# Kernel tuning notes

Measured on AMD Instinct MI355X. Metric: run time of the kernel, lower is better.

## Reference

```python
import jax, jax.numpy as jnp
import numpy as np

B, N, C, H = 32, 512, 1024, 16
HD = C // H  # head_dim = 64
SCALE = HD ** -0.5


def setup_inputs() -> dict:
    key = jax.random.key(0)
    k1, k2, k3, k4 = jax.random.split(key, 4)
    # xavier_uniform bounds
    qkv_bound = (6.0 / (C + 3 * C)) ** 0.5
    proj_bound = 1.414 * (6.0 / (C + C)) ** 0.5
    return {
        "x": jax.random.normal(k1, (B, N, C), dtype=jnp.float32),
        "mask": jax.random.uniform(k2, (B, N), dtype=jnp.float32),
        "W_qkv": jax.random.uniform(k3, (3 * C, C), dtype=jnp.float32, minval=-qkv_bound, maxval=qkv_bound),
        "W_proj": jax.random.uniform(k4, (C, C), dtype=jnp.float32, minval=-proj_bound, maxval=proj_bound),
        "b_proj": jnp.zeros((C,), dtype=jnp.float32),
    }


def reference(x, mask, W_qkv, W_proj, b_proj):
    # qkv projection (no bias): [B,N,3C] -> [3,B,H,N,HD]
    qkv = jnp.einsum("bnc,dc->bnd", x, W_qkv)
    qkv = qkv.reshape(B, N, 3, H, HD).transpose(2, 0, 3, 1, 4)
    q, k, v = qkv[0] * SCALE, qkv[1], qkv[2]
    # attention scores [B,H,N,N] with additive row/col mask bias
    attn = jnp.einsum("bhqd,bhkd->bhqk", q, k)
    attn = attn + mask[:, None, None, :] + mask[:, None, :, None]
    attn = jax.nn.softmax(attn, axis=-1)
    out = jnp.einsum("bhqk,bhkd->bhqd", attn, v)
    out = out.transpose(0, 2, 1, 3).reshape(B, N, C)
    return jnp.einsum("bnc,dc->bnd", out, W_proj) + b_proj
```

## Files before the change

kernel.cpp:

```cpp
#include <hip/hip_runtime.h>
#include <stdint.h>

typedef unsigned short u16;
typedef __bf16 bf16x8 __attribute__((ext_vector_type(8)));
typedef float  f32x4  __attribute__((ext_vector_type(4)));
typedef float  f32x16 __attribute__((ext_vector_type(16)));
typedef unsigned int u32x4 __attribute__((ext_vector_type(4)));

#define MFMA16(a,b,c) __builtin_amdgcn_mfma_f32_16x16x32_bf16((a),(b),(c),0,0,0)
#define MFMA32(a,b,c) __builtin_amdgcn_mfma_f32_32x32x16_bf16((a),(b),(c),0,0,0)

#if __has_builtin(__builtin_amdgcn_exp2f)
#define EXP2F(x) __builtin_amdgcn_exp2f(x)
#else
#define EXP2F(x) exp2f(x)
#endif

__device__ __forceinline__ u16 f2b(float f) {
  unsigned int u = __builtin_bit_cast(unsigned int, f);
  u += 0x7fffu + ((u >> 16) & 1u);
  return (u16)(u >> 16);
}

__device__ __forceinline__ void gll16(const u16* g, u16* l) {
  __builtin_amdgcn_global_load_lds((const __attribute__((address_space(1))) unsigned int*)g,
                                   (__attribute__((address_space(3))) unsigned int*)l,
                                   16, 0, 0);
}

__device__ __forceinline__ unsigned cvtpk(float lo, float hi) {
  unsigned r;
  asm("v_cvt_pk_bf16_f32 %0, %1, %2" : "=v"(r) : "v"(lo), "v"(hi));
  return r;
}
__device__ __forceinline__ void pl32swap(unsigned &x, unsigned &y) {
  asm volatile("v_permlane32_swap_b32 %0, %1" : "+v"(x), "+v"(y));
}

__global__ __launch_bounds__(256)
void cvt_all(const float* __restrict__ X, const float* __restrict__ Wq,
             const float* __restrict__ Wp, u16* __restrict__ Xb,
             u16* __restrict__ Wqb, u16* __restrict__ Wpb)
{
  size_t i = (size_t)blockIdx.x * 256 + threadIdx.x;
  const float* src; u16* dst; size_t off;
  if (i < 4194304)       { src = X;  dst = Xb;  off = i; }
  else if (i < 4980736)  { src = Wq; dst = Wqb; off = i - 4194304; }
  else                   { src = Wp; dst = Wpb; off = i - 4980736; }
  float4 v = ((const float4*)src)[off];
  uint2 p;
  p.x = f2b(v.x) | ((unsigned)f2b(v.y) << 16);
  p.y = f2b(v.z) | ((unsigned)f2b(v.w) << 16);
  ((uint2*)dst)[off] = p;
}

__global__ __launch_bounds__(256, 2)
void qkv_gemm(const u16* __restrict__ Xb, const u16* __restrict__ Wb,
              u16* __restrict__ qb, u16* __restrict__ kb, u16* __restrict__ vT)
{
  __shared__ u16 As[128 * 32];
  __shared__ u16 Bs[128 * 32];
  const int t = threadIdx.x;
  const int row0 = blockIdx.y * 128;
  const int col0 = blockIdx.x * 128;
  const int lane = t & 63, w = t >> 6;
  const int quad = lane >> 4, l16 = lane & 15;
  const int wm = w & 1, wn = w >> 1;

  f32x4 acc[4][4];
#pragma unroll
  for (int i = 0; i < 4; i++)
#pragma unroll
    for (int j = 0; j < 4; j++) acc[i][j] = f32x4{0.f, 0.f, 0.f, 0.f};

  const int srow = lane >> 2;
  const int kpart = (lane & 3) ^ ((lane >> 3) & 3);
  const u16* ga[2]; const u16* gb[2];
  u16* la[2]; u16* lb[2];
#pragma unroll
  for (int j = 0; j < 2; j++) {
    int r = w * 32 + j * 16 + srow;
    ga[j] = Xb + (size_t)(row0 + r) * 1024 + kpart * 8;
    gb[j] = Wb + (size_t)(col0 + r) * 1024 + kpart * 8;
    la[j] = As + (w * 2 + j) * 512;
    lb[j] = Bs + (w * 2 + j) * 512;
  }

  int aoff[4], boff[4];
#pragma unroll
  for (int mt = 0; mt < 4; mt++) { int r = wm * 64 + mt * 16 + l16; aoff[mt] = r * 64 + ((quad ^ ((r >> 1) & 3)) * 16); }
#pragma unroll
  for (int nt = 0; nt < 4; nt++) { int r = wn * 64 + nt * 16 + l16; boff[nt] = r * 64 + ((quad ^ ((r >> 1) & 3)) * 16); }

  for (int k0 = 0; k0 < 1024; k0 += 32) {
    __syncthreads();
#pragma unroll
    for (int j = 0; j < 2; j++) {
      gll16(ga[j] + k0, la[j]);
      gll16(gb[j] + k0, lb[j]);
    }
    __syncthreads();
    bf16x8 af[4], bfr[4];
#pragma unroll
    for (int mt = 0; mt < 4; mt++) af[mt] = *(const bf16x8*)((const char*)As + aoff[mt]);
#pragma unroll
    for (int nt = 0; nt < 4; nt++) bfr[nt] = *(const bf16x8*)((const char*)Bs + boff[nt]);
#pragma unroll
    for (int mt = 0; mt < 4; mt++)
#pragma unroll
      for (int nt = 0; nt < 4; nt++)
        acc[mt][nt] = MFMA16(af[mt], bfr[nt], acc[mt][nt]);
  }

  const int tok_base = row0 + wm * 64;
#pragma unroll
  for (int nt = 0; nt < 4; nt++) {
    int d = col0 + wn * 64 + nt * 16;
    int part = d >> 10;
    int hh = (d >> 6) & 15;
    int hd = (d & 63) + l16;
    if (part == 2) {
#pragma unroll
      for (int mt = 0; mt < 4; mt++) {
        int nb = tok_base + mt * 16 + quad * 4;
        int bb = nb >> 9, nn = nb & 511;
        uint2 pk;
        pk.x = f2b(acc[mt][nt][0]) | ((unsigned)f2b(acc[mt][nt][1]) << 16);
        pk.y = f2b(acc[mt][nt][2]) | ((unsigned)f2b(acc[mt][nt][3]) << 16);
        *(uint2*)(vT + (((size_t)(bb * 16 + hh)) * 64 + hd) * 512 + nn) = pk;
      }
    } else {
      u16* dst = (part == 0) ? qb : kb;
      float sc = (part == 0) ? 0.125f : 1.0f;
#pragma unroll
      for (int mt = 0; mt < 4; mt++)
#pragma unroll
        for (int r = 0; r < 4; r++) {
          int tok = tok_base + mt * 16 + quad * 4 + r;
          int bb = tok >> 9, nn = tok & 511;
          dst[(((size_t)(bb * 16 + hh)) * 512 + nn) * 64 + hd] = f2b(acc[mt][nt][r] * sc);
        }
    }
  }
}

__global__ __launch_bounds__(256)
void attn_kernel(const u16* __restrict__ qb, const u16* __restrict__ kb,
                 const u16* __restrict__ vT, const float* __restrict__ mask,
                 u16* __restrict__ ao)
{
  __shared__ u16 Kbuf[2][64 * 64];
  __shared__ u16 Vbuf[2][64 * 64];
  __shared__ float mk2[512];
  __shared__ float Lbuf[128];

  const int bid = blockIdx.x;
  const int wid = (bid & 7) * 256 + (bid >> 3);
  const int qt = wid & 3, bh = wid >> 2;
  const int b = bh >> 4, hh = bh & 15;

  const int t = threadIdx.x;
  const int lane = t & 63, w = t >> 6;
  const int l31 = lane & 31, hi = lane >> 5;
  const int sw = l31 & 7;

  const u16* Qp = qb + (size_t)bh * 512 * 64;
  const u16* Kp = kb + (size_t)bh * 512 * 64;
  const u16* Vp = vT + (size_t)bh * 64 * 512;

  for (int i = t; i < 512; i += 256) mk2[i] = mask[b * 512 + i] * 1.44269504f;

  const int qbase = qt * 128 + w * 32;
  bf16x8 qf[4];
#pragma unroll
  for (int dc = 0; dc < 4; dc++)
    qf[dc] = *(const bf16x8*)(Qp + (size_t)(qbase + l31) * 64 + dc * 16 + hi * 8);

  const int sr = lane >> 3, sc = lane & 7;
  const int cg = sc ^ sr;
  const u16* gk[2]; const u16* gv[2];
#pragma unroll
  for (int j = 0; j < 2; j++) {
    int r = w * 16 + j * 8 + sr;
    gk[j] = Kp + (size_t)r * 64 + cg * 8;
    gv[j] = Vp + (size_t)r * 512 + cg * 8;
  }

  f32x16 oacc[2];
#pragma unroll
  for (int i = 0; i < 16; i++) { oacc[0][i] = 0.f; oacc[1][i] = 0.f; }
  float lsum = 0.f;

  auto STAGE = [&](int tt, int buf) {
#pragma unroll
    for (int j = 0; j < 2; j++) {
      gll16(gk[j] + (size_t)tt * 4096, &Kbuf[buf][(w * 16 + j * 8) * 64]);
      gll16(gv[j] + (size_t)tt * 64,   &Vbuf[buf][(w * 16 + j * 8) * 64]);
    }
  };

  STAGE(0, 0);
  __syncthreads();

  for (int tt = 0; tt < 8; tt++) {
    const int cur = tt & 1;
    if (tt < 7) STAGE(tt + 1, cur ^ 1);
    const u16* Kb = Kbuf[cur];
    const u16* Vb = Vbuf[cur];
#pragma unroll
    for (int c = 0; c < 2; c++) {
      f32x16 s;
#pragma unroll
      for (int i = 0; i < 16; i++) s[i] = 0.f;
#pragma unroll
      for (int dc = 0; dc < 4; dc++) {
        int row = c * 32 + l31;
        bf16x8 kf = *(const bf16x8*)((const char*)Kb + row * 128 + (((2 * dc + hi) ^ sw) * 16));
        s = MFMA32(kf, qf[dc], s);
      }
      const int kb0 = tt * 64 + c * 32;
      f32x4 mkv[4];
#pragma unroll
      for (int g = 0; g < 4; g++) mkv[g] = *(const f32x4*)(mk2 + kb0 + g * 8 + hi * 4);
      float p[16];
#pragma unroll
      for (int r = 0; r < 16; r++)
        p[r] = EXP2F(fmaf(s[r], 1.44269504f, mkv[r >> 2][r & 3]));
      float ls = 0.f;
#pragma unroll
      for (int r = 0; r < 16; r++) ls += p[r];
      lsum += ls;

      unsigned d0a = cvtpk(p[0],  p[1]),  d1a = cvtpk(p[2],  p[3]);
      unsigned d2a = cvtpk(p[4],  p[5]),  d3a = cvtpk(p[6],  p[7]);
      unsigned d0b = cvtpk(p[8],  p[9]),  d1b = cvtpk(p[10], p[11]);
      unsigned d2b = cvtpk(p[12], p[13]), d3b = cvtpk(p[14], p[15]);
      pl32swap(d0a, d2a);
      pl32swap(d1a, d3a);
      pl32swap(d0b, d2b);
      pl32swap(d1b, d3b);
      u32x4 w0; w0.x = d0a; w0.y = d1a; w0.z = d2a; w0.w = d3a;
      u32x4 w1; w1.x = d0b; w1.y = d1b; w1.z = d2b; w1.w = d3b;
      bf16x8 af[2];
      af[0] = __builtin_bit_cast(bf16x8, w0);
      af[1] = __builtin_bit_cast(bf16x8, w1);

#pragma unroll
      for (int kc = 0; kc < 2; kc++)
#pragma unroll
        for (int dc = 0; dc < 2; dc++) {
          int row = dc * 32 + l31;
          bf16x8 vf = *(const bf16x8*)((const char*)Vb + row * 128 + (((4 * c + 2 * kc + hi) ^ sw) * 16));
          oacc[dc] = MFMA32(af[kc], vf, oacc[dc]);
        }
    }
    __syncthreads();
  }

  lsum += __shfl_xor(lsum, 32);
  if (lane < 32) Lbuf[w * 32 + l31] = 1.0f / lsum;
  __syncthreads();
  f32x4 inv4[4];
#pragma unroll
  for (int g = 0; g < 4; g++) inv4[g] = *(const f32x4*)(Lbuf + w * 32 + g * 8 + hi * 4);

#pragma unroll
  for (int dc = 0; dc < 2; dc++)
#pragma unroll
    for (int r = 0; r < 16; r++) {
      int qrow = (r & 3) + 8 * (r >> 2) + 4 * hi;
      int n = qbase + qrow;
      int col = hh * 64 + dc * 32 + l31;
      ao[((size_t)(b * 512 + n)) * 1024 + col] = f2b(oacc[dc][r] * inv4[r >> 2][r & 3]);
    }
}

__global__ __launch_bounds__(256, 2)
void proj_gemm(const u16* __restrict__ A, const u16* __restrict__ Wb,
               const float* __restrict__ bias, float* __restrict__ out)
{
  __shared__ u16 As[128 * 32];
  __shared__ u16 Bs[128 * 32];
  const int t = threadIdx.x;
  const int row0 = blockIdx.y * 128;
  const int col0 = blockIdx.x * 128;
  const int lane = t & 63, w = t >> 6;
  const int quad = lane >> 4, l16 = lane & 15;
  const int wm = w & 1, wn = w >> 1;

  f32x4 acc[4][4];
#pragma unroll
  for (int i = 0; i < 4; i++)
#pragma unroll
    for (int j = 0; j < 4; j++) acc[i][j] = f32x4{0.f, 0.f, 0.f, 0.f};

  const int srow = lane >> 2;
  const int kpart = (lane & 3) ^ ((lane >> 3) & 3);
  const u16* ga[2]; const u16* gb[2];
  u16* la[2]; u16* lb[2];
#pragma unroll
  for (int j = 0; j < 2; j++) {
    int r = w * 32 + j * 16 + srow;
    ga[j] = A  + (size_t)(row0 + r) * 1024 + kpart * 8;
    gb[j] = Wb + (size_t)(col0 + r) * 1024 + kpart * 8;
    la[j] = As + (w * 2 + j) * 512;
    lb[j] = Bs + (w * 2 + j) * 512;
  }

  int aoff[4], boff[4];
#pragma unroll
  for (int mt = 0; mt < 4; mt++) { int r = wm * 64 + mt * 16 + l16; aoff[mt] = r * 64 + ((quad ^ ((r >> 1) & 3)) * 16); }
#pragma unroll
  for (int nt = 0; nt < 4; nt++) { int r = wn * 64 + nt * 16 + l16; boff[nt] = r * 64 + ((quad ^ ((r >> 1) & 3)) * 16); }

  for (int k0 = 0; k0 < 1024; k0 += 32) {
    __syncthreads();
#pragma unroll
    for (int j = 0; j < 2; j++) {
      gll16(ga[j] + k0, la[j]);
      gll16(gb[j] + k0, lb[j]);
    }
    __syncthreads();
    bf16x8 af[4], bfr[4];
#pragma unroll
    for (int mt = 0; mt < 4; mt++) af[mt] = *(const bf16x8*)((const char*)As + aoff[mt]);
#pragma unroll
    for (int nt = 0; nt < 4; nt++) bfr[nt] = *(const bf16x8*)((const char*)Bs + boff[nt]);
#pragma unroll
    for (int mt = 0; mt < 4; mt++)
#pragma unroll
      for (int nt = 0; nt < 4; nt++)
        acc[mt][nt] = MFMA16(af[mt], bfr[nt], acc[mt][nt]);
  }

  const int tok_base = row0 + wm * 64;
#pragma unroll
  for (int nt = 0; nt < 4; nt++) {
    int d = col0 + wn * 64 + nt * 16 + l16;
    float bv = bias[d];
#pragma unroll
    for (int mt = 0; mt < 4; mt++)
#pragma unroll
      for (int r = 0; r < 4; r++) {
        int tok = tok_base + mt * 16 + quad * 4 + r;
        out[(size_t)tok * 1024 + d] = acc[mt][nt][r] + bv;
      }
  }
}

extern "C" void kernel_launch(void* const* d_in, const int* in_sizes, int n_in,
                              void* d_out, int out_size, void* d_ws, size_t ws_size,
                              hipStream_t stream) {
  const float* x     = (const float*)d_in[0];
  const float* mask  = (const float*)d_in[1];
  const float* Wqkv  = (const float*)d_in[2];
  const float* Wproj = (const float*)d_in[3];
  const float* bproj = (const float*)d_in[4];
  float* out = (float*)d_out;

  u16* qb  = (u16*)d_ws;
  u16* kb  = qb + 16777216;
  u16* vT  = kb + 16777216;
  u16* XbAo = vT + 16777216;
  u16* Wqb = XbAo + 16777216;
  u16* Wpb = Wqb + 3145728;

  cvt_all<<<20480, 256, 0, stream>>>(x, Wqkv, Wproj, XbAo, Wqb, Wpb);
  qkv_gemm<<<dim3(24, 128), 256, 0, stream>>>(XbAo, Wqb, qb, kb, vT);
  attn_kernel<<<2048, 256, 0, stream>>>(qb, kb, vT, mask, XbAo);
  proj_gemm<<<dim3(8, 128), 256, 0, stream>>>(XbAo, Wpb, bproj, out);
}
```

Before: 363.4 us.

## Replace QKV and proj GEMMs with 256x256 double-buffered 8-wave pipelined GEMM

Replaces both 128x128 single-buffered GEMM kernels with one templated 512-thread kernel. It uses 256x256 output tiles and K=64 double-buffered LDS, and interleaves global-to-LDS staging with LDS reads and MFMA phases using explicit barriers, waitcnts and setprio. It also remaps block ids in an XCD-aware order. The aim is to hide memory latency and raise data reuse per tile, at the cost of more registers and fewer blocks in the grid (768 and 256).

```diff
diff --git a/kernel.cpp b/kernel.cpp
--- a/kernel.cpp
+++ b/kernel.cpp
@@ -36,6 +36,12 @@
 __device__ __forceinline__ void pl32swap(unsigned &x, unsigned &y) {
   asm volatile("v_permlane32_swap_b32 %0, %1" : "+v"(x), "+v"(y));
 }
+
+#define BARR() __builtin_amdgcn_s_barrier()
+#define LGKM0() do { asm volatile("s_waitcnt lgkmcnt(0)" ::: "memory"); __builtin_amdgcn_sched_barrier(0); } while (0)
+#define VMC(N) asm volatile("s_waitcnt vmcnt(" #N ")" ::: "memory")
+#define PRIO1() __builtin_amdgcn_s_setprio(1)
+#define PRIO0() __builtin_amdgcn_s_setprio(0)
 
 __global__ __launch_bounds__(256)
 void cvt_all(const float* __restrict__ X, const float* __restrict__ Wq,
@@ -54,91 +60,171 @@
   ((uint2*)dst)[off] = p;
 }
 
-__global__ __launch_bounds__(256, 2)
-void qkv_gemm(const u16* __restrict__ Xb, const u16* __restrict__ Wb,
-              u16* __restrict__ qb, u16* __restrict__ kb, u16* __restrict__ vT)
+#define DS_A(CUR, AF, RBASE) do { \
+  _Pragma("unroll") for (int mt = 0; mt < 4; mt++) \
+  _Pragma("unroll") for (int ks = 0; ks < 2; ks++) \
+    AF[mt][ks] = *(const bf16x8*)((const char*)Asmem[CUR] + (RBASE) + aoff[mt][ks]); \
+} while (0)
+
+#define DS_B2(CUR, N0) do { \
+  _Pragma("unroll") for (int nt = 0; nt < 2; nt++) \
+  _Pragma("unroll") for (int ks = 0; ks < 2; ks++) \
+    bfr[(N0) + nt][ks] = *(const bf16x8*)((const char*)Bsmem[CUR] + boff[(N0) + nt][ks]); \
+} while (0)
+
+#define MQ(MB, NB, AF) do { \
+  _Pragma("unroll") for (int mt = 0; mt < 4; mt++) \
+  _Pragma("unroll") for (int nt = 0; nt < 2; nt++) \
+  _Pragma("unroll") for (int ks = 0; ks < 2; ks++) \
+    acc[(MB) + mt][(NB) + nt] = MFMA16(AF[mt][ks], bfr[(NB) + nt][ks], acc[(MB) + mt][(NB) + nt]); \
+} while (0)
+
+#define HALF_ITER(CUR, TA, TB, ENDW) do { \
+   \
+  DS_A(CUR, afl, 0); DS_B2(CUR, 0); \
+  STAGE_A(TA, 0); \
+  BARR(); LGKM0(); \
+  PRIO1(); MQ(0, 0, afl); PRIO0(); \
+  BARR(); \
+   \
+  DS_B2(CUR, 2); \
+  STAGE_A(TA, 1); \
+  BARR(); LGKM0(); \
+  PRIO1(); MQ(0, 2, afl); PRIO0(); \
+  BARR(); \
+   \
+  DS_A(CUR, afh, 8192); \
+  STAGE_B(TB, 0); \
+  BARR(); LGKM0(); \
+  PRIO1(); MQ(4, 0, afh); PRIO0(); \
+  BARR(); \
+   \
+  STAGE_B(TB, 1); \
+  PRIO1(); MQ(4, 2, afh); PRIO0(); \
+  ENDW; \
+  BARR(); \
+} while (0)
+
+template <int EPI>
+__global__ __launch_bounds__(512, 2)
+void gemm8p(const u16* __restrict__ Ag, const u16* __restrict__ Wg,
+            u16* __restrict__ qb, u16* __restrict__ kb, u16* __restrict__ vT,
+            const float* __restrict__ bias, float* __restrict__ outf, int nbx)
 {
-  __shared__ u16 As[128 * 32];
-  __shared__ u16 Bs[128 * 32];
+  __shared__ u16 Asmem[2][16384];
+  __shared__ u16 Bsmem[2][16384];
+
+  const int nwg = gridDim.x;
+  const int cpx = nwg >> 3;
+  const int bid = blockIdx.x;
+  const int wg  = (bid & 7) * cpx + (bid >> 3);
+  const int bx = wg % nbx, by = wg / nbx;
+  const int row0 = by * 256, col0 = bx * 256;
+
   const int t = threadIdx.x;
-  const int row0 = blockIdx.y * 128;
-  const int col0 = blockIdx.x * 128;
   const int lane = t & 63, w = t >> 6;
   const int quad = lane >> 4, l16 = lane & 15;
-  const int wm = w & 1, wn = w >> 1;
-
-  f32x4 acc[4][4];
-#pragma unroll
-  for (int i = 0; i < 4; i++)
+  const int wm = w >> 2, wn = w & 3;
+  const int sx = l16 & 7;
+
+  const int srow = lane >> 3;
+  const int scol = ((lane & 7) ^ srow) * 8;
+  const u16* pA0 = Ag + (size_t)(row0 + w * 16 + srow) * 1024 + scol;
+  const u16* pB0 = Wg + (size_t)(col0 + w * 16 + srow) * 1024 + scol;
+
+  int aoff[4][2], boff[4][2];
+#pragma unroll
+  for (int mt = 0; mt < 4; mt++)
+#pragma unroll
+    for (int ks = 0; ks < 2; ks++) {
+      int r = wm * 128 + mt * 16 + l16;
+      aoff[mt][ks] = r * 128 + (((ks * 4 + quad) ^ sx) * 16);
+    }
+#pragma unroll
+  for (int nt = 0; nt < 4; nt++)
+#pragma unroll
+    for (int ks = 0; ks < 2; ks++) {
+      int r = wn * 64 + nt * 16 + l16;
+      boff[nt][ks] = r * 128 + (((ks * 4 + quad) ^ sx) * 16);
+    }
+
+  f32x4 acc[8][4];
+#pragma unroll
+  for (int i = 0; i < 8; i++)
 #pragma unroll
     for (int j = 0; j < 4; j++) acc[i][j] = f32x4{0.f, 0.f, 0.f, 0.f};
 
-  const int srow = lane >> 2;
-  const int kpart = (lane & 3) ^ ((lane >> 3) & 3);
-  const u16* ga[2]; const u16* gb[2];
-  u16* la[2]; u16* lb[2];
-#pragma unroll
-  for (int j = 0; j < 2; j++) {
-    int r = w * 32 + j * 16 + srow;
-    ga[j] = Xb + (size_t)(row0 + r) * 1024 + kpart * 8;
-    gb[j] = Wb + (size_t)(col0 + r) * 1024 + kpart * 8;
-    la[j] = As + (w * 2 + j) * 512;
-    lb[j] = Bs + (w * 2 + j) * 512;
+  auto STAGE_A = [&](int tile, int half) {
+    if (tile >= 16) return;
+    const u16* g = pA0 + (size_t)half * 131072 + tile * 64;
+    u16* l = &Asmem[tile & 1][(half * 128 + w * 16) * 64];
+    gll16(g, l);
+    gll16(g + 8192, l + 512);
+  };
+  auto STAGE_B = [&](int tile, int half) {
+    if (tile >= 16) return;
+    const u16* g = pB0 + (size_t)half * 131072 + tile * 64;
+    u16* l = &Bsmem[tile & 1][(half * 128 + w * 16) * 64];
+    gll16(g, l);
+    gll16(g + 8192, l + 512);
+  };
+
+  bf16x8 afl[4][2], afh[4][2], bfr[4][2];
+
+  STAGE_B(0, 0); STAGE_B(0, 1); STAGE_A(0, 0); STAGE_A(0, 1);
+  STAGE_B(1, 0); STAGE_B(1, 1);
+  VMC(4); BARR();
+
+  for (int i = 0; i < 7; ++i) {
+    int t1 = 2 * i + 1;
+    HALF_ITER(0, t1, t1 + 1, VMC(4));
+    HALF_ITER(1, t1 + 1, t1 + 2, VMC(4));
   }
-
-  int aoff[4], boff[4];
-#pragma unroll
-  for (int mt = 0; mt < 4; mt++) { int r = wm * 64 + mt * 16 + l16; aoff[mt] = r * 64 + ((quad ^ ((r >> 1) & 3)) * 16); }
-#pragma unroll
-  for (int nt = 0; nt < 4; nt++) { int r = wn * 64 + nt * 16 + l16; boff[nt] = r * 64 + ((quad ^ ((r >> 1) & 3)) * 16); }
-
-  for (int k0 = 0; k0 < 1024; k0 += 32) {
-    __syncthreads();
-#pragma unroll
-    for (int j = 0; j < 2; j++) {
-      gll16(ga[j] + k0, la[j]);
-      gll16(gb[j] + k0, lb[j]);
-    }
-    __syncthreads();
-    bf16x8 af[4], bfr[4];
-#pragma unroll
-    for (int mt = 0; mt < 4; mt++) af[mt] = *(const bf16x8*)((const char*)As + aoff[mt]);
-#pragma unroll
-    for (int nt = 0; nt < 4; nt++) bfr[nt] = *(const bf16x8*)((const char*)Bs + boff[nt]);
-#pragma unroll
-    for (int mt = 0; mt < 4; mt++)
-#pragma unroll
-      for (int nt = 0; nt < 4; nt++)
-        acc[mt][nt] = MFMA16(af[mt], bfr[nt], acc[mt][nt]);
-  }
-
-  const int tok_base = row0 + wm * 64;
-#pragma unroll
-  for (int nt = 0; nt < 4; nt++) {
-    int d = col0 + wn * 64 + nt * 16;
-    int part = d >> 10;
-    int hh = (d >> 6) & 15;
-    int hd = (d & 63) + l16;
-    if (part == 2) {
-#pragma unroll
-      for (int mt = 0; mt < 4; mt++) {
-        int nb = tok_base + mt * 16 + quad * 4;
-        int bb = nb >> 9, nn = nb & 511;
-        uint2 pk;
-        pk.x = f2b(acc[mt][nt][0]) | ((unsigned)f2b(acc[mt][nt][1]) << 16);
-        pk.y = f2b(acc[mt][nt][2]) | ((unsigned)f2b(acc[mt][nt][3]) << 16);
-        *(uint2*)(vT + (((size_t)(bb * 16 + hh)) * 64 + hd) * 512 + nn) = pk;
+  HALF_ITER(0, 15, 16, VMC(0));
+  HALF_ITER(1, 16, 17, ((void)0));
+
+  const int tok_base = row0 + wm * 128;
+  if constexpr (EPI == 0) {
+#pragma unroll
+    for (int nt = 0; nt < 4; nt++) {
+      int d = col0 + wn * 64 + nt * 16;
+      int part = d >> 10;
+      int hh = (d >> 6) & 15;
+      int hd = (d & 63) + l16;
+      if (part == 2) {
+#pragma unroll
+        for (int mt = 0; mt < 8; mt++) {
+          int nb = tok_base + mt * 16 + quad * 4;
+          int bb = nb >> 9, nn = nb & 511;
+          uint2 pk;
+          pk.x = f2b(acc[mt][nt][0]) | ((unsigned)f2b(acc[mt][nt][1]) << 16);
+          pk.y = f2b(acc[mt][nt][2]) | ((unsigned)f2b(acc[mt][nt][3]) << 16);
+          *(uint2*)(vT + (((size_t)(bb * 16 + hh)) * 64 + hd) * 512 + nn) = pk;
+        }
+      } else {
+        u16* dst = (part == 0) ? qb : kb;
+        float sc = (part == 0) ? 0.125f : 1.0f;
+#pragma unroll
+        for (int mt = 0; mt < 8; mt++)
+#pragma unroll
+          for (int r = 0; r < 4; r++) {
+            int tok = tok_base + mt * 16 + quad * 4 + r;
+            int bb = tok >> 9, nn = tok & 511;
+            dst[(((size_t)(bb * 16 + hh)) * 512 + nn) * 64 + hd] = f2b(acc[mt][nt][r] * sc);
+          }
       }
-    } else {
-      u16* dst = (part == 0) ? qb : kb;
-      float sc = (part == 0) ? 0.125f : 1.0f;
-#pragma unroll
-      for (int mt = 0; mt < 4; mt++)
+    }
+  } else {
+#pragma unroll
+    for (int nt = 0; nt < 4; nt++) {
+      int d = col0 + wn * 64 + nt * 16 + l16;
+      float bv = bias[d];
+#pragma unroll
+      for (int mt = 0; mt < 8; mt++)
 #pragma unroll
         for (int r = 0; r < 4; r++) {
           int tok = tok_base + mt * 16 + quad * 4 + r;
-          int bb = tok >> 9, nn = tok & 511;
-          dst[(((size_t)(bb * 16 + hh)) * 512 + nn) * 64 + hd] = f2b(acc[mt][nt][r] * sc);
+          outf[(size_t)tok * 1024 + d] = acc[mt][nt][r] + bv;
         }
     }
   }
@@ -275,79 +361,6 @@
     }
 }
 
-__global__ __launch_bounds__(256, 2)
-void proj_gemm(const u16* __restrict__ A, const u16* __restrict__ Wb,
-               const float* __restrict__ bias, float* __restrict__ out)
-{
-  __shared__ u16 As[128 * 32];
-  __shared__ u16 Bs[128 * 32];
-  const int t = threadIdx.x;
-  const int row0 = blockIdx.y * 128;
-  const int col0 = blockIdx.x * 128;
-  const int lane = t & 63, w = t >> 6;
-  const int quad = lane >> 4, l16 = lane & 15;
-  const int wm = w & 1, wn = w >> 1;
-
-  f32x4 acc[4][4];
-#pragma unroll
-  for (int i = 0; i < 4; i++)
-#pragma unroll
-    for (int j = 0; j < 4; j++) acc[i][j] = f32x4{0.f, 0.f, 0.f, 0.f};
-
-  const int srow = lane >> 2;
-  const int kpart = (lane & 3) ^ ((lane >> 3) & 3);
-  const u16* ga[2]; const u16* gb[2];
-  u16* la[2]; u16* lb[2];
-#pragma unroll
-  for (int j = 0; j < 2; j++) {
-    int r = w * 32 + j * 16 + srow;
-    ga[j] = A  + (size_t)(row0 + r) * 1024 + kpart * 8;
-    gb[j] = Wb + (size_t)(col0 + r) * 1024 + kpart * 8;
-    la[j] = As + (w * 2 + j) * 512;
-    lb[j] = Bs + (w * 2 + j) * 512;
-  }
-
-  int aoff[4], boff[4];
-#pragma unroll
-  for (int mt = 0; mt < 4; mt++) { int r = wm * 64 + mt * 16 + l16; aoff[mt] = r * 64 + ((quad ^ ((r >> 1) & 3)) * 16); }
-#pragma unroll
-  for (int nt = 0; nt < 4; nt++) { int r = wn * 64 + nt * 16 + l16; boff[nt] = r * 64 + ((quad ^ ((r >> 1) & 3)) * 16); }
-
-  for (int k0 = 0; k0 < 1024; k0 += 32) {
-    __syncthreads();
-#pragma unroll
-    for (int j = 0; j < 2; j++) {
-      gll16(ga[j] + k0, la[j]);
-      gll16(gb[j] + k0, lb[j]);
-    }
-    __syncthreads();
-    bf16x8 af[4], bfr[4];
-#pragma unroll
-    for (int mt = 0; mt < 4; mt++) af[mt] = *(const bf16x8*)((const char*)As + aoff[mt]);
-#pragma unroll
-    for (int nt = 0; nt < 4; nt++) bfr[nt] = *(const bf16x8*)((const char*)Bs + boff[nt]);
-#pragma unroll
-    for (int mt = 0; mt < 4; mt++)
-#pragma unroll
-      for (int nt = 0; nt < 4; nt++)
-        acc[mt][nt] = MFMA16(af[mt], bfr[nt], acc[mt][nt]);
-  }
-
-  const int tok_base = row0 + wm * 64;
-#pragma unroll
-  for (int nt = 0; nt < 4; nt++) {
-    int d = col0 + wn * 64 + nt * 16 + l16;
-    float bv = bias[d];
-#pragma unroll
-    for (int mt = 0; mt < 4; mt++)
-#pragma unroll
-      for (int r = 0; r < 4; r++) {
-        int tok = tok_base + mt * 16 + quad * 4 + r;
-        out[(size_t)tok * 1024 + d] = acc[mt][nt][r] + bv;
-      }
-  }
-}
-
 extern "C" void kernel_launch(void* const* d_in, const int* in_sizes, int n_in,
                               void* d_out, int out_size, void* d_ws, size_t ws_size,
                               hipStream_t stream) {
@@ -366,7 +379,7 @@
   u16* Wpb = Wqb + 3145728;
 
   cvt_all<<<20480, 256, 0, stream>>>(x, Wqkv, Wproj, XbAo, Wqb, Wpb);
-  qkv_gemm<<<dim3(24, 128), 256, 0, stream>>>(XbAo, Wqb, qb, kb, vT);
+  gemm8p<0><<<768, 512, 0, stream>>>(XbAo, Wqb, qb, kb, vT, nullptr, nullptr, 12);
   attn_kernel<<<2048, 256, 0, stream>>>(qb, kb, vT, mask, XbAo);
-  proj_gemm<<<dim3(8, 128), 256, 0, stream>>>(XbAo, Wpb, bproj, out);
-}
+  gemm8p<1><<<256, 512, 0, stream>>>(XbAo, Wpb, nullptr, nullptr, nullptr, bproj, out, 4);
+}
```

Result: faster. 340.3 us (-6.4%).
